# Performance work log

Hardware: AMD Instinct MI355X
Metric: run time of the kernel (lower is better)

Reference implementation:

```python
import jax, jax.numpy as jnp
import numpy as np

B, S, D, H, DEPTH, VOCAB = 4096, 64, 512, 8, 4, 2
HD = D // H
EPS = 1e-5


def setup_inputs() -> dict:
    key = jax.random.key(0)
    ks = jax.random.split(key, 12)
    sc = 0.02
    return {
        "a_seq": jax.random.randint(ks[0], (B, S), 0, VOCAB, dtype=jnp.int32),
        "b_seq": jax.random.randint(ks[1], (B, S), 0, VOCAB, dtype=jnp.int32),
        "bit_emb": jax.random.normal(ks[2], (VOCAB, D), jnp.float32),
        "start_state": jax.random.normal(ks[3], (D,), jnp.float32),
        "ln1_g": jnp.ones((DEPTH, D), jnp.float32),
        "ln1_b": jnp.zeros((DEPTH, D), jnp.float32),
        # weights stored [in, out] (transpose of torch nn.Linear layout)
        "qkv_w": jax.random.normal(ks[4], (DEPTH, D, 3 * D), jnp.float32) * sc,
        "qkv_b": jnp.zeros((DEPTH, 3 * D), jnp.float32),
        "out_w": jax.random.normal(ks[5], (DEPTH, D, D), jnp.float32) * sc,
        "out_b": jnp.zeros((DEPTH, D), jnp.float32),
        "ln2_g": jnp.ones((DEPTH, D), jnp.float32),
        "ln2_b": jnp.zeros((DEPTH, D), jnp.float32),
        "ff1_w": jax.random.normal(ks[6], (DEPTH, D, 4 * D), jnp.float32) * sc,
        "ff1_b": jnp.zeros((DEPTH, 4 * D), jnp.float32),
        "ff2_w": jax.random.normal(ks[7], (DEPTH, 4 * D, D), jnp.float32) * sc,
        "ff2_b": jnp.zeros((DEPTH, D), jnp.float32),
        "head_w": jax.random.normal(ks[8], (D, 2), jnp.float32) * sc,
        "head_b": jnp.zeros((2,), jnp.float32),
    }


def _ln(x, g, b):
    m = x.mean(-1, keepdims=True)
    c = x - m
    v = (c * c).mean(-1, keepdims=True)
    return c * jax.lax.rsqrt(v + EPS) * g + b


def reference(a_seq, b_seq, bit_emb, start_state, ln1_g, ln1_b, qkv_w, qkv_b,
              out_w, out_b, ln2_g, ln2_b, ff1_w, ff1_b, ff2_w, ff2_b,
              head_w, head_b):
    # [B,S,D] combined bit embeddings, then time-major for scan
    emb = bit_emb[a_seq] + bit_emb[b_seq]
    xs = jnp.swapaxes(emb, 0, 1)  # [S,B,D]
    h0 = jnp.broadcast_to(start_state, (a_seq.shape[0], D))

    def step(h, xt):
        x = xt + h  # current_input = emb_a + emb_b + h_t, [B,D] (seq_len=1 squeezed)
        for l in range(DEPTH):  # pre-norm TransformerEncoderLayer, norm_first=True
            y = _ln(x, ln1_g[l], ln1_b[l])
            qkv = y @ qkv_w[l] + qkv_b[l]
            # self-attention over a single token: softmax of one score == 1,
            # so the attention output is exactly V (grads to Q,K are zero, as in torch)
            v = qkv[:, 2 * D:]
            x = x + v @ out_w[l] + out_b[l]
            y = _ln(x, ln2_g[l], ln2_b[l])
            x = x + jax.nn.relu(y @ ff1_w[l] + ff1_b[l]) @ ff2_w[l] + ff2_b[l]
        return x, x @ head_w + head_b

    _, logits = jax.lax.scan(step, h0, xs)  # [S,B,2]
    return jnp.swapaxes(logits, 0, 1)  # [B,S,2]
```

## Files before the change

kernel.cpp:

```cpp
#include <hip/hip_runtime.h>
#include <hip/hip_bf16.h>
#include <stdint.h>
#include <stddef.h>

#define B_ 4096
#define S_ 64
#define D_ 512
#define DEPTH_ 4


typedef __attribute__((ext_vector_type(8))) __bf16 bf16x8;
typedef __attribute__((ext_vector_type(4))) float f32x4;
typedef __hip_bfloat16 bf16_t;

__device__ __forceinline__ void async_copy16(const void* g, void* lds) {
  __builtin_amdgcn_global_load_lds(
      (const __attribute__((address_space(1))) void*)g,
      (__attribute__((address_space(3))) void*)lds, 16, 0, 0);
}

__device__ __forceinline__ float bf2f(bf16_t h) { return __bfloat162float(h); }

template<int TM, int TN, int EPI, int SPLITK>
__launch_bounds__(256)
__global__ void gemm_bf16(const bf16_t* __restrict__ A,
                          const bf16_t* __restrict__ Bt,
                          const float* __restrict__ bias,
                          bf16_t* __restrict__ O,
                          int M, int N, int K)
{
  constexpr int BK  = 64;
  constexpr int WM  = TM / 2, WN = TN / 2;
  constexpr int NMI = WM / 16, NNI = WN / 16;
  constexpr int CA  = TM / 8, CB = TN / 8;

  __shared__ __align__(16) bf16_t sA[TM * BK];
  __shared__ __align__(16) bf16_t sB[TN * BK];

  const int tid  = threadIdx.x;
  const int lane = tid & 63;
  const int wave = tid >> 6;
  const int wm   = wave & 1;
  const int wn   = wave >> 1;
  const int m0   = blockIdx.x * TM;
  const int n0   = blockIdx.y * TN;
  const int KS   = K / SPLITK;
  const int kbeg = blockIdx.z * KS;

  const int lr = lane >> 3;
  const int lc = (lane & 7) * 8;

  f32x4 acc[NMI][NNI];
#pragma unroll
  for (int mi = 0; mi < NMI; ++mi)
#pragma unroll
    for (int ni = 0; ni < NNI; ++ni)
      acc[mi][ni] = (f32x4){0.f, 0.f, 0.f, 0.f};

  for (int k0 = kbeg; k0 < kbeg + KS; k0 += BK) {
#pragma unroll
    for (int c = wave; c < CA; c += 4) {
      const bf16_t* g = A + (size_t)(m0 + c * 8 + lr) * K + (k0 + lc);
      async_copy16(g, (char*)sA + c * 1024);
    }
#pragma unroll
    for (int c = wave; c < CB; c += 4) {
      const bf16_t* g = Bt + (size_t)(n0 + c * 8 + lr) * K + (k0 + lc);
      async_copy16(g, (char*)sB + c * 1024);
    }
    __syncthreads();

#pragma unroll
    for (int kk = 0; kk < BK; kk += 32) {
      bf16x8 af[NMI], bfv[NNI];
#pragma unroll
      for (int mi = 0; mi < NMI; ++mi)
        af[mi] = *(const bf16x8*)&sA[(wm * WM + mi * 16 + (lane & 15)) * BK + kk + (lane >> 4) * 8];
#pragma unroll
      for (int ni = 0; ni < NNI; ++ni)
        bfv[ni] = *(const bf16x8*)&sB[(wn * WN + ni * 16 + (lane & 15)) * BK + kk + (lane >> 4) * 8];
#pragma unroll
      for (int mi = 0; mi < NMI; ++mi)
#pragma unroll
        for (int ni = 0; ni < NNI; ++ni)
          acc[mi][ni] = __builtin_amdgcn_mfma_f32_16x16x32_bf16(af[mi], bfv[ni], acc[mi][ni], 0, 0, 0);
    }
    __syncthreads();
  }

#pragma unroll
  for (int mi = 0; mi < NMI; ++mi) {
#pragma unroll
    for (int ni = 0; ni < NNI; ++ni) {
      const int col  = n0 + wn * WN + ni * 16 + (lane & 15);
      const int row0 = m0 + wm * WM + mi * 16 + ((lane >> 4) << 2);
      const float bv = (SPLITK == 1 || blockIdx.z == 0) ? bias[col] : 0.f;
#pragma unroll
      for (int r = 0; r < 4; ++r) {
        const float v = acc[mi][ni][r] + bv;
        const size_t idx = (size_t)(row0 + r) * N + col;
        if constexpr (EPI == 1) {
          O[idx] = __float2bfloat16(v > 0.f ? v : 0.f);
        } else {
          O[(size_t)blockIdx.z * M * N + idx] = __float2bfloat16(v);
        }
      }
    }
  }
}

__device__ __forceinline__ void ln_store(const float v[8],
                                         const float* __restrict__ gamma,
                                         const float* __restrict__ beta,
                                         bf16_t* __restrict__ yrow, int lane)
{
  float s = 0.f, ss = 0.f;
#pragma unroll
  for (int i = 0; i < 8; ++i) { s += v[i]; ss += v[i] * v[i]; }
#pragma unroll
  for (int o = 32; o; o >>= 1) { s += __shfl_xor(s, o); ss += __shfl_xor(ss, o); }
  const float m   = s * (1.f / D_);
  const float inv = rsqrtf(ss * (1.f / D_) - m * m + 1e-5f);
  const int c0 = lane * 8;
  float g[8], b[8];
  *(float4*)&g[0] = *(const float4*)&gamma[c0];
  *(float4*)&g[4] = *(const float4*)&gamma[c0 + 4];
  *(float4*)&b[0] = *(const float4*)&beta[c0];
  *(float4*)&b[4] = *(const float4*)&beta[c0 + 4];
  alignas(16) bf16_t o8[8];
#pragma unroll
  for (int i = 0; i < 8; ++i)
    o8[i] = __float2bfloat16((v[i] - m) * inv * g[i] + b[i]);
  *(uint4*)&yrow[c0] = *(const uint4*)o8;
}

__device__ __forceinline__ void fold_p(float v[8], const bf16_t* pz)
{
  alignas(16) bf16_t t[8];
  *(uint4*)t = *(const uint4*)pz;
#pragma unroll
  for (int i = 0; i < 8; ++i) v[i] += bf2f(t[i]);
}

template<int NZ>
__global__ void ln_sumN_kernel(float* __restrict__ X,
                               const bf16_t* __restrict__ P,
                               const float* __restrict__ gamma,
                               const float* __restrict__ beta,
                               bf16_t* __restrict__ Y)
{
  const int row  = blockIdx.x * 4 + (threadIdx.x >> 6);
  const int lane = threadIdx.x & 63;
  const int c0 = lane * 8;
  float* xr = X + (size_t)row * D_;
  float v[8];
  *(float4*)&v[0] = *(const float4*)&xr[c0];
  *(float4*)&v[4] = *(const float4*)&xr[c0 + 4];
#pragma unroll
  for (int z = 0; z < NZ; ++z)
    fold_p(v, P + (size_t)z * B_ * D_ + (size_t)row * D_ + c0);
  *(float4*)&xr[c0]     = *(const float4*)&v[0];
  *(float4*)&xr[c0 + 4] = *(const float4*)&v[4];
  ln_store(v, gamma, beta, Y + (size_t)row * D_, lane);
}

__global__ void add_ln_kernel(const int* __restrict__ a_seq,
                              const int* __restrict__ b_seq,
                              const float* __restrict__ bit_emb,
                              const float* __restrict__ hsrc, int hstride,
                              const bf16_t* __restrict__ P,
                              float* __restrict__ X,
                              const float* __restrict__ gamma,
                              const float* __restrict__ beta,
                              bf16_t* __restrict__ Y, int t,
                              const float* __restrict__ hw,
                              const float* __restrict__ hb,
                              float* __restrict__ out)
{
  const int row  = blockIdx.x * 4 + (threadIdx.x >> 6);
  const int lane = threadIdx.x & 63;
  const int ai = a_seq[row * S_ + t];
  const int bi = b_seq[row * S_ + t];
  const int c0 = lane * 8;
  float* xr = X + (size_t)row * D_;
  const float* pr = hsrc + (size_t)row * hstride + c0;
  float ea[8], eb[8], p[8], v[8];
  *(float4*)&ea[0] = *(const float4*)&bit_emb[ai * D_ + c0];
  *(float4*)&ea[4] = *(const float4*)&bit_emb[ai * D_ + c0 + 4];
  *(float4*)&eb[0] = *(const float4*)&bit_emb[bi * D_ + c0];
  *(float4*)&eb[4] = *(const float4*)&bit_emb[bi * D_ + c0 + 4];
  *(float4*)&p[0]  = *(const float4*)&pr[0];
  *(float4*)&p[4]  = *(const float4*)&pr[4];

  if (P != nullptr) {
#pragma unroll
    for (int z = 0; z < 4; ++z)
      fold_p(p, P + (size_t)z * B_ * D_ + (size_t)row * D_ + c0);
  }

  if (out != nullptr) {
    float w[16];
#pragma unroll
    for (int i = 0; i < 4; ++i)
      *(float4*)&w[i * 4] = *(const float4*)&hw[lane * 16 + i * 4];
    float s0 = 0.f, s1 = 0.f;
#pragma unroll
    for (int i = 0; i < 8; ++i) { s0 += p[i] * w[2 * i]; s1 += p[i] * w[2 * i + 1]; }
#pragma unroll
    for (int o = 32; o; o >>= 1) { s0 += __shfl_xor(s0, o); s1 += __shfl_xor(s1, o); }
    if (lane == 0) {
      float* po = out + (size_t)row * (S_ * 2) + (t - 1) * 2;
      po[0] = s0 + hb[0];
      po[1] = s1 + hb[1];
    }
  }

#pragma unroll
  for (int i = 0; i < 8; ++i) v[i] = ea[i] + eb[i] + p[i];
  *(float4*)&xr[c0]     = *(const float4*)&v[0];
  *(float4*)&xr[c0 + 4] = *(const float4*)&v[4];
  ln_store(v, gamma, beta, Y + (size_t)row * D_, lane);
}

__global__ void head_kernel(const float* __restrict__ X,
                            const bf16_t* __restrict__ P,
                            const float* __restrict__ hw,
                            const float* __restrict__ hb,
                            float* __restrict__ out, int t)
{
  const int row  = blockIdx.x * 4 + (threadIdx.x >> 6);
  const int lane = threadIdx.x & 63;
  const float* xr = X + (size_t)row * D_;
  const int c0 = lane * 8;
  float v[8];
  *(float4*)&v[0] = *(const float4*)&xr[c0];
  *(float4*)&v[4] = *(const float4*)&xr[c0 + 4];
#pragma unroll
  for (int z = 0; z < 4; ++z)
    fold_p(v, P + (size_t)z * B_ * D_ + (size_t)row * D_ + c0);
  float w[16];
#pragma unroll
  for (int i = 0; i < 4; ++i)
    *(float4*)&w[i * 4] = *(const float4*)&hw[lane * 16 + i * 4];
  float s0 = 0.f, s1 = 0.f;
#pragma unroll
  for (int i = 0; i < 8; ++i) { s0 += v[i] * w[2 * i]; s1 += v[i] * w[2 * i + 1]; }
#pragma unroll
  for (int o = 32; o; o >>= 1) { s0 += __shfl_xor(s0, o); s1 += __shfl_xor(s1, o); }
  if (lane == 0) {
    float* po = out + (size_t)row * (S_ * 2) + t * 2;
    po[0] = s0 + hb[0];
    po[1] = s1 + hb[1];
  }
}

__global__ void prep_wc(const float* __restrict__ qkv_w,
                        const float* __restrict__ out_w,
                        float* __restrict__ wc)
{
  const int n = blockIdx.x * 256 + threadIdx.x;
  const int k = blockIdx.y;
  const int l = blockIdx.z;
  const float* qrow = qkv_w + ((size_t)l * D_ + k) * (3 * D_) + 2 * D_;
  const float* ow   = out_w + (size_t)l * D_ * D_;
  float acc = 0.f;
  for (int j = 0; j < D_; ++j) acc += qrow[j] * ow[(size_t)j * D_ + n];
  wc[((size_t)l * D_ + k) * D_ + n] = acc;
}

__global__ void prep_bc(const float* __restrict__ qkv_b,
                        const float* __restrict__ out_w,
                        const float* __restrict__ out_b,
                        float* __restrict__ bc)
{
  const int l = blockIdx.x;
  const int n = threadIdx.x;
  const float* qb = qkv_b + (size_t)l * (3 * D_) + 2 * D_;
  const float* ow = out_w + (size_t)l * D_ * D_;
  float acc = out_b[(size_t)l * D_ + n];
  for (int j = 0; j < D_; ++j) acc += qb[j] * ow[(size_t)j * D_ + n];
  bc[(size_t)l * D_ + n] = acc;
}

__global__ void transpose_conv(const float* __restrict__ src,
                               bf16_t* __restrict__ dst, int R, int C)
{
  __shared__ float tile[32][33];
  const int l = blockIdx.z;
  const float* s = src + (size_t)l * R * C;
  bf16_t* d = dst + (size_t)l * R * C;
  const int c0 = blockIdx.x * 32, r0 = blockIdx.y * 32;
  const int tx = threadIdx.x, ty = threadIdx.y;
  tile[ty][tx] = s[(size_t)(r0 + ty) * C + (c0 + tx)];
  __syncthreads();
  d[(size_t)(c0 + ty) * R + (r0 + tx)] = __float2bfloat16(tile[tx][ty]);
}

extern "C" void kernel_launch(void* const* d_in, const int* in_sizes, int n_in,
                              void* d_out, int out_size, void* d_ws, size_t ws_size,
                              hipStream_t stream)
{
  const int*   a_seq     = (const int*)  d_in[0];
  const int*   b_seq     = (const int*)  d_in[1];
  const float* bit_emb   = (const float*)d_in[2];
  const float* start     = (const float*)d_in[3];
  const float* ln1_g     = (const float*)d_in[4];
  const float* ln1_b     = (const float*)d_in[5];
  const float* qkv_w     = (const float*)d_in[6];
  const float* qkv_b     = (const float*)d_in[7];
  const float* out_w     = (const float*)d_in[8];
  const float* out_b     = (const float*)d_in[9];
  const float* ln2_g     = (const float*)d_in[10];
  const float* ln2_b     = (const float*)d_in[11];
  const float* ff1_w     = (const float*)d_in[12];
  const float* ff1_b     = (const float*)d_in[13];
  const float* ff2_w     = (const float*)d_in[14];
  const float* ff2_b     = (const float*)d_in[15];
  const float* head_w    = (const float*)d_in[16];
  const float* head_b    = (const float*)d_in[17];
  float* out = (float*)d_out;

  char* ws = (char*)d_ws;
  float*  X     = (float*) ws; ws += (size_t)B_ * D_ * 4;
  bf16_t* Y     = (bf16_t*)ws; ws += (size_t)B_ * D_ * 2;
  bf16_t* U     = (bf16_t*)ws; ws += (size_t)B_ * 4 * D_ * 2;
  bf16_t* WCT   = (bf16_t*)ws; ws += (size_t)DEPTH_ * D_ * D_ * 2;
  bf16_t* FF1T  = (bf16_t*)ws; ws += (size_t)DEPTH_ * D_ * 4 * D_ * 2;
  bf16_t* FF2T  = (bf16_t*)ws; ws += (size_t)DEPTH_ * 4 * D_ * D_ * 2;
  float*  BC    = (float*) ws; ws += (size_t)DEPTH_ * D_ * 4;
  float*  WCTMP = (float*) ws; ws += (size_t)DEPTH_ * D_ * D_ * 4;
  bf16_t* PSPL  = (bf16_t*)ws; ws += (size_t)4 * B_ * D_ * 2;
  bf16_t* P1    = (bf16_t*)ws; ws += (size_t)B_ * D_ * 2;

  prep_wc<<<dim3(2, 512, 4), 256, 0, stream>>>(qkv_w, out_w, WCTMP);
  prep_bc<<<4, 512, 0, stream>>>(qkv_b, out_w, out_b, BC);
  transpose_conv<<<dim3(16, 16, 4),  dim3(32, 32), 0, stream>>>(WCTMP, WCT, 512, 512);
  transpose_conv<<<dim3(64, 16, 4),  dim3(32, 32), 0, stream>>>(ff1_w, FF1T, 512, 2048);
  transpose_conv<<<dim3(16, 64, 4),  dim3(32, 32), 0, stream>>>(ff2_w, FF2T, 2048, 512);

  for (int t = 0; t < S_; ++t) {
    if (t == 0)
      add_ln_kernel<<<B_ / 4, 256, 0, stream>>>(a_seq, b_seq, bit_emb, start, 0,
                                                nullptr, X, ln1_g, ln1_b, Y, t,
                                                head_w, head_b, nullptr);
    else
      add_ln_kernel<<<B_ / 4, 256, 0, stream>>>(a_seq, b_seq, bit_emb, X, D_,
                                                PSPL, X, ln1_g, ln1_b, Y, t,
                                                head_w, head_b, out);
    for (int l = 0; l < DEPTH_; ++l) {
      gemm_bf16<64, 64, 2, 1><<<dim3(64, 8), 256, 0, stream>>>(
          Y, WCT + (size_t)l * D_ * D_, BC + (size_t)l * D_, P1,
          B_, D_, D_);
      ln_sumN_kernel<1><<<B_ / 4, 256, 0, stream>>>(X, P1,
                                                    ln2_g + (size_t)l * D_,
                                                    ln2_b + (size_t)l * D_, Y);
      gemm_bf16<128, 128, 1, 1><<<dim3(32, 16), 256, 0, stream>>>(
          Y, FF1T + (size_t)l * D_ * 4 * D_, ff1_b + (size_t)l * 4 * D_, U,
          B_, 4 * D_, D_);
      gemm_bf16<128, 128, 2, 4><<<dim3(32, 4, 4), 256, 0, stream>>>(
          U, FF2T + (size_t)l * 4 * D_ * D_, ff2_b + (size_t)l * D_, PSPL,
          B_, D_, 4 * D_);
      if (l < DEPTH_ - 1)
        ln_sumN_kernel<4><<<B_ / 4, 256, 0, stream>>>(X, PSPL,
                                                      ln1_g + (size_t)(l + 1) * D_,
                                                      ln1_b + (size_t)(l + 1) * D_, Y);
    }
  }
  head_kernel<<<B_ / 4, 256, 0, stream>>>(X, PSPL, head_w, head_b, out, S_ - 1);
}
```

Measured before the change: 15.13 ms.

## Fuse split-K fold and LayerNorm into combined V/out GEMM; stage GEMM epilogue via LDS

For layers 1 to 3, a new lnfold_gemm kernel sums the four split-K FF2 partials into the residual, applies LN1 into LDS, and runs the folded V/out-projection GEMM from there. This replaces a separate ln_sumN<4> kernel and the round trip of Y through global memory. The residual ping-pongs between XA and XB, because each block reads the old X while block y==0 writes the new one. Separately, the generic GEMM epilogue now stages the bf16 C tile in reused LDS so it can write coalesced 16-byte stores. The cost is that the fold and LN work is recomputed in each of the 4 column blocks, and the fused kernel has small tiles with no double buffering.

```diff
diff --git a/kernel.cpp b/kernel.cpp
--- a/kernel.cpp
+++ b/kernel.cpp
@@ -33,9 +33,11 @@
   constexpr int WM  = TM / 2, WN = TN / 2;
   constexpr int NMI = WM / 16, NNI = WN / 16;
   constexpr int CA  = TM / 8, CB = TN / 8;
-
-  __shared__ __align__(16) bf16_t sA[TM * BK];
-  __shared__ __align__(16) bf16_t sB[TN * BK];
+  static_assert(TM * TN <= (TM + TN) * BK, "C tile must fit in staging LDS");
+
+  __shared__ __align__(16) bf16_t smem[(TM + TN) * BK];
+  bf16_t* sA = smem;
+  bf16_t* sB = smem + TM * BK;
 
   const int tid  = threadIdx.x;
   const int lane = tid & 63;
@@ -88,31 +90,37 @@
     __syncthreads();
   }
 
+  bf16_t* sC = smem;
 #pragma unroll
   for (int mi = 0; mi < NMI; ++mi) {
 #pragma unroll
     for (int ni = 0; ni < NNI; ++ni) {
-      const int col  = n0 + wn * WN + ni * 16 + (lane & 15);
-      const int row0 = m0 + wm * WM + mi * 16 + ((lane >> 4) << 2);
-      const float bv = (SPLITK == 1 || blockIdx.z == 0) ? bias[col] : 0.f;
+      const int col  = wn * WN + ni * 16 + (lane & 15);
+      const int row0 = wm * WM + mi * 16 + ((lane >> 4) << 2);
+      const float bv = (SPLITK == 1 || blockIdx.z == 0) ? bias[n0 + col] : 0.f;
 #pragma unroll
       for (int r = 0; r < 4; ++r) {
-        const float v = acc[mi][ni][r] + bv;
-        const size_t idx = (size_t)(row0 + r) * N + col;
-        if constexpr (EPI == 1) {
-          O[idx] = __float2bfloat16(v > 0.f ? v : 0.f);
-        } else {
-          O[(size_t)blockIdx.z * M * N + idx] = __float2bfloat16(v);
-        }
+        float v = acc[mi][ni][r] + bv;
+        if constexpr (EPI == 1) v = v > 0.f ? v : 0.f;
+        sC[(row0 + r) * TN + col] = __float2bfloat16(v);
       }
     }
+  }
+  __syncthreads();
+  bf16_t* Ob = O + (EPI == 2 ? (size_t)blockIdx.z * M * N : (size_t)0);
+#pragma unroll
+  for (int p = 0; p < (TM * TN) / 2048; ++p) {
+    const int chunk = p * 256 + tid;
+    const int rr = chunk / (TN / 8);
+    const int cc = (chunk % (TN / 8)) * 8;
+    *(uint4*)&Ob[(size_t)(m0 + rr) * N + n0 + cc] = *(const uint4*)&sC[rr * TN + cc];
   }
 }
 
 __device__ __forceinline__ void ln_store(const float v[8],
                                          const float* __restrict__ gamma,
                                          const float* __restrict__ beta,
-                                         bf16_t* __restrict__ yrow, int lane)
+                                         bf16_t* yrow, int lane)
 {
   float s = 0.f, ss = 0.f;
 #pragma unroll
@@ -162,6 +170,103 @@
   *(float4*)&xr[c0]     = *(const float4*)&v[0];
   *(float4*)&xr[c0 + 4] = *(const float4*)&v[4];
   ln_store(v, gamma, beta, Y + (size_t)row * D_, lane);
+}
+
+__launch_bounds__(256)
+__global__ void lnfold_gemm(const float* __restrict__ Xin,
+                            const bf16_t* __restrict__ P,
+                            float* __restrict__ Xout,
+                            const float* __restrict__ gamma,
+                            const float* __restrict__ beta,
+                            const bf16_t* __restrict__ Bt,
+                            const float* __restrict__ bias,
+                            bf16_t* __restrict__ O)
+{
+  constexpr int TM = 32, TN = 128, BK = 64;
+  __shared__ __align__(16) bf16_t sY[TM * D_];
+  __shared__ __align__(16) bf16_t sB[TN * BK];
+
+  const int tid  = threadIdx.x;
+  const int lane = tid & 63;
+  const int wave = tid >> 6;
+  const int m0   = blockIdx.x * TM;
+  const int n0   = blockIdx.y * TN;
+  const int c0   = lane * 8;
+
+#pragma unroll
+  for (int i = 0; i < 8; ++i) {
+    const int row  = wave * 8 + i;
+    const int grow = m0 + row;
+    const float* xr = Xin + (size_t)grow * D_ + c0;
+    float v[8];
+    *(float4*)&v[0] = *(const float4*)&xr[0];
+    *(float4*)&v[4] = *(const float4*)&xr[4];
+#pragma unroll
+    for (int z = 0; z < 4; ++z)
+      fold_p(v, P + (size_t)z * B_ * D_ + (size_t)grow * D_ + c0);
+    if (blockIdx.y == 0) {
+      float* xo = Xout + (size_t)grow * D_ + c0;
+      *(float4*)&xo[0] = *(const float4*)&v[0];
+      *(float4*)&xo[4] = *(const float4*)&v[4];
+    }
+    ln_store(v, gamma, beta, &sY[row * D_], lane);
+  }
+
+  f32x4 acc[2][2];
+#pragma unroll
+  for (int mi = 0; mi < 2; ++mi)
+#pragma unroll
+    for (int ni = 0; ni < 2; ++ni)
+      acc[mi][ni] = (f32x4){0.f, 0.f, 0.f, 0.f};
+
+  const int lr = lane >> 3;
+  const int lc = (lane & 7) * 8;
+  for (int k0 = 0; k0 < D_; k0 += BK) {
+#pragma unroll
+    for (int c = wave; c < TN / 8; c += 4) {
+      const bf16_t* g = Bt + (size_t)(n0 + c * 8 + lr) * D_ + (k0 + lc);
+      async_copy16(g, (char*)sB + c * 1024);
+    }
+    __syncthreads();
+#pragma unroll
+    for (int kk = 0; kk < BK; kk += 32) {
+      bf16x8 af[2], bfv[2];
+#pragma unroll
+      for (int mi = 0; mi < 2; ++mi)
+        af[mi] = *(const bf16x8*)&sY[(mi * 16 + (lane & 15)) * D_ + k0 + kk + (lane >> 4) * 8];
+#pragma unroll
+      for (int ni = 0; ni < 2; ++ni)
+        bfv[ni] = *(const bf16x8*)&sB[(wave * 32 + ni * 16 + (lane & 15)) * BK + kk + (lane >> 4) * 8];
+#pragma unroll
+      for (int mi = 0; mi < 2; ++mi)
+#pragma unroll
+        for (int ni = 0; ni < 2; ++ni)
+          acc[mi][ni] = __builtin_amdgcn_mfma_f32_16x16x32_bf16(af[mi], bfv[ni], acc[mi][ni], 0, 0, 0);
+    }
+    __syncthreads();
+  }
+
+  bf16_t* sC = sY;
+#pragma unroll
+  for (int mi = 0; mi < 2; ++mi) {
+#pragma unroll
+    for (int ni = 0; ni < 2; ++ni) {
+      const int col  = wave * 32 + ni * 16 + (lane & 15);
+      const int row0 = mi * 16 + ((lane >> 4) << 2);
+      const float bv = bias[n0 + col];
+#pragma unroll
+      for (int r = 0; r < 4; ++r)
+        sC[(row0 + r) * TN + col] = __float2bfloat16(acc[mi][ni][r] + bv);
+    }
+  }
+  __syncthreads();
+#pragma unroll
+  for (int p = 0; p < (TM * TN) / 2048; ++p) {
+    const int chunk = p * 256 + tid;
+    const int rr = chunk / (TN / 8);
+    const int cc = (chunk % (TN / 8)) * 8;
+    *(uint4*)&O[(size_t)(m0 + rr) * D_ + n0 + cc] = *(const uint4*)&sC[rr * TN + cc];
+  }
 }
 
 __global__ void add_ln_kernel(const int* __restrict__ a_seq,
@@ -321,7 +426,7 @@
   float* out = (float*)d_out;
 
   char* ws = (char*)d_ws;
-  float*  X     = (float*) ws; ws += (size_t)B_ * D_ * 4;
+  float*  XA    = (float*) ws; ws += (size_t)B_ * D_ * 4;
   bf16_t* Y     = (bf16_t*)ws; ws += (size_t)B_ * D_ * 2;
   bf16_t* U     = (bf16_t*)ws; ws += (size_t)B_ * 4 * D_ * 2;
   bf16_t* WCT   = (bf16_t*)ws; ws += (size_t)DEPTH_ * D_ * D_ * 2;
@@ -331,6 +436,7 @@
   float*  WCTMP = (float*) ws; ws += (size_t)DEPTH_ * D_ * D_ * 4;
   bf16_t* PSPL  = (bf16_t*)ws; ws += (size_t)4 * B_ * D_ * 2;
   bf16_t* P1    = (bf16_t*)ws; ws += (size_t)B_ * D_ * 2;
+  float*  XB    = (float*) ws; ws += (size_t)B_ * D_ * 4;
 
   prep_wc<<<dim3(2, 512, 4), 256, 0, stream>>>(qkv_w, out_w, WCTMP);
   prep_bc<<<4, 512, 0, stream>>>(qkv_b, out_w, out_b, BC);
@@ -341,17 +447,28 @@
   for (int t = 0; t < S_; ++t) {
     if (t == 0)
       add_ln_kernel<<<B_ / 4, 256, 0, stream>>>(a_seq, b_seq, bit_emb, start, 0,
-                                                nullptr, X, ln1_g, ln1_b, Y, t,
+                                                nullptr, XA, ln1_g, ln1_b, Y, t,
                                                 head_w, head_b, nullptr);
     else
-      add_ln_kernel<<<B_ / 4, 256, 0, stream>>>(a_seq, b_seq, bit_emb, X, D_,
-                                                PSPL, X, ln1_g, ln1_b, Y, t,
+      add_ln_kernel<<<B_ / 4, 256, 0, stream>>>(a_seq, b_seq, bit_emb, XB, D_,
+                                                PSPL, XA, ln1_g, ln1_b, Y, t,
                                                 head_w, head_b, out);
     for (int l = 0; l < DEPTH_; ++l) {
-      gemm_bf16<64, 64, 2, 1><<<dim3(64, 8), 256, 0, stream>>>(
-          Y, WCT + (size_t)l * D_ * D_, BC + (size_t)l * D_, P1,
-          B_, D_, D_);
-      ln_sumN_kernel<1><<<B_ / 4, 256, 0, stream>>>(X, P1,
+      float* Xcur;
+      if (l == 0) {
+        gemm_bf16<64, 64, 2, 1><<<dim3(64, 8), 256, 0, stream>>>(
+            Y, WCT, BC, P1, B_, D_, D_);
+        Xcur = XA;
+      } else {
+        float* Xin  = (l & 1) ? XA : XB;
+        float* Xout = (l & 1) ? XB : XA;
+        lnfold_gemm<<<dim3(B_ / 32, 4), 256, 0, stream>>>(
+            Xin, PSPL, Xout,
+            ln1_g + (size_t)l * D_, ln1_b + (size_t)l * D_,
+            WCT + (size_t)l * D_ * D_, BC + (size_t)l * D_, P1);
+        Xcur = Xout;
+      }
+      ln_sumN_kernel<1><<<B_ / 4, 256, 0, stream>>>(Xcur, P1,
                                                     ln2_g + (size_t)l * D_,
                                                     ln2_b + (size_t)l * D_, Y);
       gemm_bf16<128, 128, 1, 1><<<dim3(32, 16), 256, 0, stream>>>(
@@ -360,11 +477,7 @@
       gemm_bf16<128, 128, 2, 4><<<dim3(32, 4, 4), 256, 0, stream>>>(
           U, FF2T + (size_t)l * 4 * D_ * D_, ff2_b + (size_t)l * D_, PSPL,
           B_, D_, 4 * D_);
-      if (l < DEPTH_ - 1)
-        ln_sumN_kernel<4><<<B_ / 4, 256, 0, stream>>>(X, PSPL,
-                                                      ln1_g + (size_t)(l + 1) * D_,
-                                                      ln1_b + (size_t)(l + 1) * D_, Y);
-    }
-  }
-  head_kernel<<<B_ / 4, 256, 0, stream>>>(X, PSPL, head_w, head_b, out, S_ - 1);
-}
+    }
+  }
+  head_kernel<<<B_ / 4, 256, 0, stream>>>(XB, PSPL, head_w, head_b, out, S_ - 1);
+}
```

New measurement: 14.91 ms. Within noise of the previous version (-1.5%).
